# Performance work log

Measured on AMD Instinct MI355X. Metric: run time of the kernel, lower is better.

Reference implementation:

```python
import jax, jax.numpy as jnp
import numpy as np

NEG_SLOPE = 0.2  # PyG GATv2Conv default leaky_relu slope


def _gatv2(x, src, dst, eattr, Wl, bl, Wr, br, We, att, bias, N):
    """GATv2Conv (concat heads, eval mode -> no dropout).
    x: [N, Fin], src/dst: [E], eattr: [E, Fe], att: [H, C]."""
    H, C = att.shape
    xl = (x @ Wl.T + bl).reshape(N, H, C)   # lin_l -> source features
    xr = (x @ Wr.T + br).reshape(N, H, C)   # lin_r -> target features
    ea = (eattr @ We.T).reshape(-1, H, C)   # lin_edge (no bias)
    m = xl[src] + xr[dst] + ea              # [E, H, C]
    m = jnp.where(m >= 0, m, NEG_SLOPE * m)
    logits = jnp.einsum('ehc,hc->eh', m, att)  # [E, H]
    # segment softmax over incoming edges of each target node
    lmax = jax.ops.segment_max(logits, dst, num_segments=N)  # self-loops -> nonempty
    ex = jnp.exp(logits - lmax[dst])
    denom = jax.ops.segment_sum(ex, dst, num_segments=N)
    alpha = ex / denom[dst]                 # [E, H]
    out = jax.ops.segment_sum(alpha[:, :, None] * xl[src], dst, num_segments=N)
    return out.reshape(N, H * C) + bias


def setup_inputs() -> dict:
    key = jax.random.key(0)
    ks = jax.random.split(key, 24)
    B, num_nodes, Fn, Fe, deg = 16, 5000, 64, 16, 32
    N = B * num_nodes
    E = N * deg
    s = 0.05
    inp = {
        'x': jax.random.normal(ks[0], (N, Fn), jnp.float32),
        'edge_index': jax.random.randint(ks[1], (2, E), 0, N, jnp.int64),
        'edge_attr': jax.random.normal(ks[2], (E, Fe), jnp.float32),
        'num_nodes': num_nodes,
        'W1l': jax.random.normal(ks[3], (9, Fn), jnp.float32) * s,
        'b1l': jnp.zeros((9,), jnp.float32),
        'W1r': jax.random.normal(ks[4], (9, Fn), jnp.float32) * s,
        'b1r': jnp.zeros((9,), jnp.float32),
        'We1': jax.random.normal(ks[5], (9, Fe), jnp.float32) * s,
        'att1': jax.random.normal(ks[6], (3, 3), jnp.float32) * s,
        'bias1': jnp.zeros((9,), jnp.float32),
        'W2l': jax.random.normal(ks[7], (20, 9), jnp.float32) * s,
        'b2l': jnp.zeros((20,), jnp.float32),
        'W2r': jax.random.normal(ks[8], (20, 9), jnp.float32) * s,
        'b2r': jnp.zeros((20,), jnp.float32),
        'We2': jax.random.normal(ks[9], (20, Fe), jnp.float32) * s,
        'att2': jax.random.normal(ks[10], (4, 5), jnp.float32) * s,
        'bias2': jnp.zeros((20,), jnp.float32),
        'fcW1': jax.random.normal(ks[11], (100, 20 * num_nodes), jnp.float32) * 0.01,
        'fcb1': jnp.zeros((100,), jnp.float32),
        'fcW2': jax.random.normal(ks[12], (10, 100), jnp.float32) * s,
        'fcb2': jnp.zeros((10,), jnp.float32),
        'fcW3': jax.random.normal(ks[13], (1, 10), jnp.float32) * s,
        'fcb3': jnp.zeros((1,), jnp.float32),
    }
    return inp


def reference(x, edge_index, edge_attr, num_nodes,
              W1l, b1l, W1r, b1r, We1, att1, bias1,
              W2l, b2l, W2r, b2r, We2, att2, bias2,
              fcW1, fcb1, fcW2, fcb2, fcW3, fcb3):
    N = x.shape[0]
    src0, dst0 = edge_index[0], edge_index[1]
    # add_self_loops=True, fill_value='mean': loop attr = mean of incoming edge attrs
    cnt = jax.ops.segment_sum(jnp.ones((src0.shape[0],), x.dtype), dst0, num_segments=N)
    loop_attr = jax.ops.segment_sum(edge_attr, dst0, num_segments=N) / jnp.maximum(cnt, 1.0)[:, None]
    nodes = jnp.arange(N)
    src = jnp.concatenate([src0, nodes])
    dst = jnp.concatenate([dst0, nodes])
    ea = jnp.concatenate([edge_attr, loop_attr], axis=0)

    h = _gatv2(x, src, dst, ea, W1l, b1l, W1r, b1r, We1, att1, bias1, N)
    h = jax.nn.relu(h)
    h = _gatv2(h, src, dst, ea, W2l, b2l, W2r, b2r, We2, att2, bias2, N)
    h = jax.nn.relu(h)

    B = N // num_nodes
    h = h.reshape(B, num_nodes * 20)
    h = jax.nn.relu(h @ fcW1.T + fcb1)
    h = jax.nn.relu(h @ fcW2.T + fcb2)
    return h @ fcW3.T + fcb3
```

## Files before the change

kernel.cpp:

```cpp
#include <hip/hip_runtime.h>
#include <math.h>

#define TPB 256
#define CAP 96
#define CPAD 16

static inline int gridFor(size_t n) { return (int)((n + TPB - 1) / TPB); }


__global__ void __launch_bounds__(TPB) k_lin1(
    const float* __restrict__ x,
    const float* __restrict__ Wl, const float* __restrict__ bl,
    const float* __restrict__ Wr, const float* __restrict__ br,
    float* __restrict__ xl, float* __restrict__ xr, int N)
{
  int idx = blockIdx.x * TPB + threadIdx.x;
  if (idx >= N * 18) return;
  int i = idx / 18, t = idx % 18;
  bool left = t < 9;
  int j = left ? t : t - 9;
  const float* W = (left ? Wl : Wr) + j * 64;
  float s = (left ? bl : br)[j];
  const float* xi = x + (size_t)i * 64;
#pragma unroll
  for (int f = 0; f < 64; f++) s = fmaf(xi[f], W[f], s);
  (left ? xl : xr)[(size_t)i * 9 + j] = s;
}

__global__ void __launch_bounds__(TPB) k_lin2(
    const float* __restrict__ h1, const float* __restrict__ bias1,
    const float* __restrict__ Wl, const float* __restrict__ bl,
    const float* __restrict__ Wr, const float* __restrict__ br,
    float* __restrict__ xl, float* __restrict__ xr, int N)
{
  int idx = blockIdx.x * TPB + threadIdx.x;
  if (idx >= N * 40) return;
  int i = idx / 40, t = idx % 40;
  float hr[9];
#pragma unroll
  for (int k = 0; k < 9; k++) hr[k] = fmaxf(h1[(size_t)i * 9 + k] + bias1[k], 0.0f);
  bool left = t < 20;
  int j = left ? t : t - 20;
  const float* W = (left ? Wl : Wr) + j * 9;
  float s = (left ? bl : br)[j];
#pragma unroll
  for (int k = 0; k < 9; k++) s = fmaf(hr[k], W[k], s);
  (left ? xl : xr)[(size_t)i * 20 + j] = s;
}


__global__ void __launch_bounds__(TPB) k_scatter(
    const int* __restrict__ ei, int* __restrict__ cursor,
    int2* __restrict__ csr, int E)
{
  size_t e = (size_t)blockIdx.x * TPB + threadIdx.x;
  if (e >= (size_t)E) return;
  int src = ei[e];
  int dst = ei[(size_t)E + e];
  int slot = atomicAdd(&cursor[(size_t)dst * CPAD], 1);
  if (slot < CAP) csr[(size_t)dst * CAP + slot] = make_int2((int)e, src);
}


template <int H, int C>
__global__ void __launch_bounds__(TPB) k_attn(
    const int* __restrict__ cursor, const int2* __restrict__ csr,
    const float* __restrict__ eattr,
    const float* __restrict__ xl, const float* __restrict__ xr,
    const float* __restrict__ We, const float* __restrict__ att,
    const float* __restrict__ bias,
    float* __restrict__ out, int N)
{
  constexpr int HC = H * C;
  int idx = blockIdx.x * TPB + threadIdx.x;
  if (idx >= N * H) return;
  int n = idx / H, h = idx % H;

  float w[C][16];
#pragma unroll
  for (int c = 0; c < C; c++)
#pragma unroll
    for (int f = 0; f < 16; f++) w[c][f] = We[(h * C + c) * 16 + f];
  float attv[C], xrv[C];
#pragma unroll
  for (int c = 0; c < C; c++) {
    attv[c] = att[h * C + c];
    xrv[c] = xr[(size_t)n * HC + h * C + c];
  }

  int dg = cursor[(size_t)n * CPAD];
  int lim = min(dg, CAP);
  const int2* row = csr + (size_t)n * CAP;

  float mx = -INFINITY, den = 0.0f;
  float acc[C], ea_sum[C];
#pragma unroll
  for (int c = 0; c < C; c++) { acc[c] = 0.0f; ea_sum[c] = 0.0f; }

  for (int p = 0; p < lim; p++) {
    int2 es = row[p];
    float a[16];
    const float4* a4 = (const float4*)(eattr + (size_t)es.x * 16);
#pragma unroll
    for (int k = 0; k < 4; k++) {
      float4 v = a4[k];
      a[4 * k + 0] = v.x; a[4 * k + 1] = v.y; a[4 * k + 2] = v.z; a[4 * k + 3] = v.w;
    }
    const float* xs = xl + (size_t)es.y * HC + h * C;
    float xv[C];
#pragma unroll
    for (int c = 0; c < C; c++) xv[c] = xs[c];
    float lg = 0.0f;
#pragma unroll
    for (int c = 0; c < C; c++) {
      float ea = 0.0f;
#pragma unroll
      for (int f = 0; f < 16; f++) ea = fmaf(a[f], w[c][f], ea);
      ea_sum[c] += ea;
      float m = xv[c] + xrv[c] + ea;
      m = (m >= 0.0f) ? m : 0.2f * m;
      lg = fmaf(m, attv[c], lg);
    }
    float nm = fmaxf(mx, lg);
    float s = expf(mx - nm);
    float wE = expf(lg - nm);
    den = den * s + wE;
#pragma unroll
    for (int c = 0; c < C; c++) acc[c] = fmaf(acc[c], s, wE * xv[c]);
    mx = nm;
  }

  {
    float invd = 1.0f / fmaxf((float)dg, 1.0f);
    const float* xs = xl + (size_t)n * HC + h * C;
    float xv[C];
#pragma unroll
    for (int c = 0; c < C; c++) xv[c] = xs[c];
    float lg = 0.0f;
#pragma unroll
    for (int c = 0; c < C; c++) {
      float m = xv[c] + xrv[c] + ea_sum[c] * invd;
      m = (m >= 0.0f) ? m : 0.2f * m;
      lg = fmaf(m, attv[c], lg);
    }
    float nm = fmaxf(mx, lg);
    float s = expf(mx - nm);
    float wE = expf(lg - nm);
    den = den * s + wE;
#pragma unroll
    for (int c = 0; c < C; c++) acc[c] = fmaf(acc[c], s, wE * xv[c]);
  }

  float inv = 1.0f / den;
  float* od = out + (size_t)n * HC + h * C;
#pragma unroll
  for (int c = 0; c < C; c++) {
    float v = acc[c] * inv;
    if (bias) v = fmaxf(v + bias[h * C + c], 0.0f);
    od[c] = v;
  }
}


__global__ void __launch_bounds__(TPB) k_fc1(
    const float* __restrict__ h2, const float* __restrict__ W,
    float* __restrict__ h3, int NN, int Kc)
{
  int o = blockIdx.x;
  int ks = blockIdx.y;
  int k0 = ks * Kc;
  int k1 = min(NN, k0 + Kc);
  float acc[16];
#pragma unroll
  for (int b = 0; b < 16; b++) acc[b] = 0.0f;
  const float* wo = W + (size_t)o * NN;
  for (int k = k0 + threadIdx.x; k < k1; k += TPB) {
    float w = wo[k];
#pragma unroll
    for (int b = 0; b < 16; b++) acc[b] = fmaf(h2[(size_t)b * NN + k], w, acc[b]);
  }
#pragma unroll
  for (int b = 0; b < 16; b++) {
    float v = acc[b];
#pragma unroll
    for (int off = 32; off > 0; off >>= 1) v += __shfl_down(v, off, 64);
    if ((threadIdx.x & 63) == 0) atomicAdd(&h3[b * 100 + o], v);
  }
}

__global__ void __launch_bounds__(TPB) k_fc23(
    const float* __restrict__ h3, const float* __restrict__ fcb1,
    const float* __restrict__ W2, const float* __restrict__ b2,
    const float* __restrict__ W3, const float* __restrict__ b3,
    float* __restrict__ out, int B)
{
  __shared__ float s3[32 * 100];
  __shared__ float s4[32 * 10];
  int tid = threadIdx.x;
  for (int t = tid; t < B * 100; t += TPB)
    s3[t] = fmaxf(h3[t] + fcb1[t % 100], 0.0f);
  __syncthreads();
  if (tid < B * 10) {
    int b = tid / 10, o = tid % 10;
    float s = b2[o];
#pragma unroll
    for (int k = 0; k < 100; k++) s = fmaf(s3[b * 100 + k], W2[o * 100 + k], s);
    s4[tid] = fmaxf(s, 0.0f);
  }
  __syncthreads();
  if (tid < B) {
    float s = b3[0];
#pragma unroll
    for (int k = 0; k < 10; k++) s = fmaf(s4[tid * 10 + k], W3[k], s);
    out[tid] = s;
  }
}


extern "C" void kernel_launch(void* const* d_in, const int* in_sizes, int n_in,
                              void* d_out, int out_size, void* d_ws, size_t ws_size,
                              hipStream_t stream) {
  const float* x      = (const float*)d_in[0];
  const int*   ei     = (const int*)d_in[1];
  const float* eattr  = (const float*)d_in[2];
  const float* W1l = (const float*)d_in[4];  const float* b1l = (const float*)d_in[5];
  const float* W1r = (const float*)d_in[6];  const float* b1r = (const float*)d_in[7];
  const float* We1 = (const float*)d_in[8];  const float* att1 = (const float*)d_in[9];
  const float* bias1 = (const float*)d_in[10];
  const float* W2l = (const float*)d_in[11]; const float* b2l = (const float*)d_in[12];
  const float* W2r = (const float*)d_in[13]; const float* b2r = (const float*)d_in[14];
  const float* We2 = (const float*)d_in[15]; const float* att2 = (const float*)d_in[16];
  const float* bias2 = (const float*)d_in[17];
  const float* fcW1 = (const float*)d_in[18]; const float* fcb1 = (const float*)d_in[19];
  const float* fcW2 = (const float*)d_in[20]; const float* fcb2 = (const float*)d_in[21];
  const float* fcW3 = (const float*)d_in[22]; const float* fcb3 = (const float*)d_in[23];
  float* out = (float*)d_out;

  const int N = in_sizes[0] / 64;
  const int E = in_sizes[2] / 16;
  const int num_nodes = in_sizes[18] / (100 * 20);
  const int B = N / num_nodes;

  char* base = (char*)d_ws;
  size_t off = 0;
  auto alloc = [&](size_t bytes) {
    size_t o = off; off += (bytes + 63) & ~(size_t)63; return o;
  };
  size_t o_cursor = alloc((size_t)N * CPAD * 4);
  size_t o_h3     = alloc((size_t)B * 100 * 4);
  size_t zeroBytes = off;
  size_t o_csr    = alloc((size_t)N * CAP * 8);
  size_t o_xl1    = alloc((size_t)N * 9 * 4);
  size_t o_xr1    = alloc((size_t)N * 9 * 4);
  size_t o_xl2    = alloc((size_t)N * 20 * 4);
  size_t o_xr2    = alloc((size_t)N * 20 * 4);
  size_t o_h1     = alloc((size_t)N * 9 * 4);
  size_t o_h2     = alloc((size_t)N * 20 * 4);
  (void)ws_size;

  int*   cursor = (int*)(base + o_cursor);
  float* h3     = (float*)(base + o_h3);
  int2*  csr    = (int2*)(base + o_csr);
  float* xl1    = (float*)(base + o_xl1);
  float* xr1    = (float*)(base + o_xr1);
  float* xl2    = (float*)(base + o_xl2);
  float* xr2    = (float*)(base + o_xr2);
  float* h1     = (float*)(base + o_h1);
  float* h2     = (float*)(base + o_h2);

  hipMemsetAsync(d_ws, 0, zeroBytes, stream);

  k_lin1<<<gridFor((size_t)N * 18), TPB, 0, stream>>>(x, W1l, b1l, W1r, b1r, xl1, xr1, N);

  k_scatter<<<gridFor((size_t)E), TPB, 0, stream>>>(ei, cursor, csr, E);

  k_attn<3, 3><<<gridFor((size_t)N * 3), TPB, 0, stream>>>(
      cursor, csr, eattr, xl1, xr1, We1, att1, nullptr, h1, N);

  k_lin2<<<gridFor((size_t)N * 40), TPB, 0, stream>>>(h1, bias1, W2l, b2l, W2r, b2r, xl2, xr2, N);

  k_attn<4, 5><<<gridFor((size_t)N * 4), TPB, 0, stream>>>(
      cursor, csr, eattr, xl2, xr2, We2, att2, bias2, h2, N);

  const int NN = num_nodes * 20;
  const int KS = 16;
  const int Kc = (NN + KS - 1) / KS;
  dim3 g1(100, KS);
  k_fc1<<<g1, TPB, 0, stream>>>(h2, fcW1, h3, NN, Kc);
  k_fc23<<<1, TPB, 0, stream>>>(h3, fcb1, fcW2, fcb2, fcW3, fcb3, out, B);
  (void)out_size; (void)n_in;
}
```

Measured before the change: 856.5 us.

## Build compact CSR via two-level bucket sort and reorder edge attributes

Replaces the per-node atomic slot scatter into a fixed-capacity padded CSR with a two-level binning scheme. Edges are binned by destination block using shared-memory histograms, bucket offsets are scanned, and a per-bucket kernel builds a compact rowptr/src/eid CSR. When workspace allows, edge attributes are permuted into CSR order so the attention kernels read them sequentially instead of gathering by edge id. This adds several kernels and a full copy of the edge attributes. It relies on fixed bucket capacity (BCAP) and on edge ids fitting in 22 bits.

New measurement: 832.4 us. -2.8%, faster.

```diff
diff --git a/kernel.cpp b/kernel.cpp
--- a/kernel.cpp
+++ b/kernel.cpp
@@ -1,9 +1,12 @@
 #include <hip/hip_runtime.h>
 #include <math.h>
 
-#define TPB 256
-#define CAP 96
-#define CPAD 16
+#define TPB   256
+#define NPB   256
+#define MAXNB 512
+#define BCAP  10240
+#define ITEMS 32
+#define CPAD  16
 
 static inline int gridFor(size_t n) { return (int)((n + TPB - 1) / TPB); }
 
@@ -49,23 +52,122 @@
 }
 
 
-__global__ void __launch_bounds__(TPB) k_scatter(
-    const int* __restrict__ ei, int* __restrict__ cursor,
-    int2* __restrict__ csr, int E)
-{
-  size_t e = (size_t)blockIdx.x * TPB + threadIdx.x;
-  if (e >= (size_t)E) return;
-  int src = ei[e];
-  int dst = ei[(size_t)E + e];
-  int slot = atomicAdd(&cursor[(size_t)dst * CPAD], 1);
-  if (slot < CAP) csr[(size_t)dst * CAP + slot] = make_int2((int)e, src);
-}
-
-
-template <int H, int C>
+__global__ void __launch_bounds__(TPB) k_bin(
+    const int* __restrict__ ei, int* __restrict__ bucketCntP,
+    int2* __restrict__ staging, int E, int NB)
+{
+  __shared__ int hist[MAXNB];
+  __shared__ int base[MAXNB];
+  int tid = threadIdx.x;
+  size_t tile0 = (size_t)blockIdx.x * (TPB * ITEMS);
+  for (int i = tid; i < NB; i += TPB) hist[i] = 0;
+  __syncthreads();
+  for (int it = 0; it < ITEMS; ++it) {
+    size_t e = tile0 + (size_t)it * TPB + tid;
+    if (e < (size_t)E) {
+      int dst = ei[(size_t)E + e];
+      atomicAdd(&hist[dst >> 8], 1);
+    }
+  }
+  __syncthreads();
+  for (int i = tid; i < NB; i += TPB) {
+    int c = hist[i];
+    base[i] = c ? atomicAdd(&bucketCntP[(size_t)i * CPAD], c) : 0;
+    hist[i] = 0;
+  }
+  __syncthreads();
+  for (int it = 0; it < ITEMS; ++it) {
+    size_t e = tile0 + (size_t)it * TPB + tid;
+    if (e < (size_t)E) {
+      int src = ei[e];
+      int dst = ei[(size_t)E + e];
+      int b = dst >> 8;
+      int r = atomicAdd(&hist[b], 1);
+      staging[(size_t)b * BCAP + base[b] + r] =
+          make_int2((int)e | ((dst & 255) << 22), src);
+    }
+  }
+}
+
+
+__global__ void __launch_bounds__(MAXNB) k_scanb(
+    const int* __restrict__ bucketCntP, int* __restrict__ bucketBase, int NB)
+{
+  __shared__ int s[MAXNB];
+  int tid = threadIdx.x;
+  int v = (tid < NB) ? bucketCntP[(size_t)tid * CPAD] : 0;
+  s[tid] = v;
+  __syncthreads();
+  for (int off = 1; off < MAXNB; off <<= 1) {
+    int u = (tid >= off) ? s[tid - off] : 0;
+    __syncthreads();
+    s[tid] += u;
+    __syncthreads();
+  }
+  if (tid < NB) bucketBase[tid] = s[tid] - v;
+}
+
+
+__global__ void __launch_bounds__(TPB) k_csr(
+    const int2* __restrict__ staging, const int* __restrict__ bucketCntP,
+    const int* __restrict__ bucketBase,
+    int* __restrict__ rowptr, int* __restrict__ degO,
+    int* __restrict__ src_csr, int* __restrict__ eid_csr, int N)
+{
+  int b = blockIdx.x, tid = threadIdx.x;
+  int n0 = b << 8;
+  int recCnt = bucketCntP[(size_t)b * CPAD];
+  int ebase = bucketBase[b];
+  const int2* rec = staging + (size_t)b * BCAP;
+  __shared__ int deg_s[NPB];
+  __shared__ int pfx[NPB];
+  __shared__ int cur[NPB];
+  deg_s[tid] = 0;
+  __syncthreads();
+  for (int r = tid; r < recCnt; r += TPB)
+    atomicAdd(&deg_s[(rec[r].x >> 22) & 255], 1);
+  __syncthreads();
+  pfx[tid] = deg_s[tid];
+  __syncthreads();
+  for (int off = 1; off < NPB; off <<= 1) {
+    int u = (tid >= off) ? pfx[tid - off] : 0;
+    __syncthreads();
+    pfx[tid] += u;
+    __syncthreads();
+  }
+  int excl = pfx[tid] - deg_s[tid];
+  int n = n0 + tid;
+  if (n < N) { rowptr[n] = ebase + excl; degO[n] = deg_s[tid]; }
+  cur[tid] = ebase + excl;
+  __syncthreads();
+  for (int r = tid; r < recCnt; r += TPB) {
+    int2 rc = rec[r];
+    int dl = (rc.x >> 22) & 255;
+    int eid = rc.x & 0x3FFFFF;
+    int pos = atomicAdd(&cur[dl], 1);
+    src_csr[pos] = rc.y;
+    eid_csr[pos] = eid;
+  }
+}
+
+
+__global__ void __launch_bounds__(TPB) k_reorder(
+    const int* __restrict__ eid_csr, const float* __restrict__ eattr,
+    float4* __restrict__ eac, int E)
+{
+  int slot = blockIdx.x * TPB + threadIdx.x;
+  if (slot >= E) return;
+  const float4* s = (const float4*)(eattr + (size_t)eid_csr[slot] * 16);
+  float4* d = eac + (size_t)slot * 4;
+  d[0] = s[0]; d[1] = s[1]; d[2] = s[2]; d[3] = s[3];
+}
+
+
+template <int H, int C, bool SEQ>
 __global__ void __launch_bounds__(TPB) k_attn(
-    const int* __restrict__ cursor, const int2* __restrict__ csr,
-    const float* __restrict__ eattr,
+    const int* __restrict__ rowptr, const int* __restrict__ deg,
+    const int* __restrict__ src_csr, const int* __restrict__ eid_csr,
+    const float* __restrict__ ea_src,
     const float* __restrict__ xl, const float* __restrict__ xr,
     const float* __restrict__ We, const float* __restrict__ att,
     const float* __restrict__ bias,
@@ -88,25 +190,26 @@
     xrv[c] = xr[(size_t)n * HC + h * C + c];
   }
 
-  int dg = cursor[(size_t)n * CPAD];
-  int lim = min(dg, CAP);
-  const int2* row = csr + (size_t)n * CAP;
+  int r0 = rowptr[n];
+  int dg = deg[n];
 
   float mx = -INFINITY, den = 0.0f;
   float acc[C], ea_sum[C];
 #pragma unroll
   for (int c = 0; c < C; c++) { acc[c] = 0.0f; ea_sum[c] = 0.0f; }
 
-  for (int p = 0; p < lim; p++) {
-    int2 es = row[p];
+  for (int p = 0; p < dg; p++) {
+    int pos = r0 + p;
+    size_t abase = SEQ ? (size_t)pos * 16 : (size_t)eid_csr[pos] * 16;
     float a[16];
-    const float4* a4 = (const float4*)(eattr + (size_t)es.x * 16);
+    const float4* a4 = (const float4*)(ea_src + abase);
 #pragma unroll
     for (int k = 0; k < 4; k++) {
       float4 v = a4[k];
       a[4 * k + 0] = v.x; a[4 * k + 1] = v.y; a[4 * k + 2] = v.z; a[4 * k + 3] = v.w;
     }
-    const float* xs = xl + (size_t)es.y * HC + h * C;
+    int srcn = src_csr[pos];
+    const float* xs = xl + (size_t)srcn * HC + h * C;
     float xv[C];
 #pragma unroll
     for (int c = 0; c < C; c++) xv[c] = xs[c];
@@ -240,47 +343,73 @@
   const int E = in_sizes[2] / 16;
   const int num_nodes = in_sizes[18] / (100 * 20);
   const int B = N / num_nodes;
+  const int NB = (N + NPB - 1) / NPB;
 
   char* base = (char*)d_ws;
   size_t off = 0;
   auto alloc = [&](size_t bytes) {
     size_t o = off; off += (bytes + 63) & ~(size_t)63; return o;
   };
-  size_t o_cursor = alloc((size_t)N * CPAD * 4);
+  size_t o_bcnt   = alloc((size_t)NB * CPAD * 4);
   size_t o_h3     = alloc((size_t)B * 100 * 4);
   size_t zeroBytes = off;
-  size_t o_csr    = alloc((size_t)N * CAP * 8);
+  size_t o_bbase  = alloc((size_t)NB * 4);
+  size_t o_stage  = alloc((size_t)NB * BCAP * 8);
+  size_t o_rowptr = alloc((size_t)N * 4);
+  size_t o_deg    = alloc((size_t)N * 4);
+  size_t o_srcc   = alloc((size_t)E * 4);
+  size_t o_eidc   = alloc((size_t)E * 4);
   size_t o_xl1    = alloc((size_t)N * 9 * 4);
   size_t o_xr1    = alloc((size_t)N * 9 * 4);
   size_t o_xl2    = alloc((size_t)N * 20 * 4);
   size_t o_xr2    = alloc((size_t)N * 20 * 4);
   size_t o_h1     = alloc((size_t)N * 9 * 4);
   size_t o_h2     = alloc((size_t)N * 20 * 4);
-  (void)ws_size;
-
-  int*   cursor = (int*)(base + o_cursor);
+  size_t o_eac    = alloc((size_t)E * 16 * 4);
+  bool seq = (off <= ws_size);
+
+  int*   bcnt   = (int*)(base + o_bcnt);
   float* h3     = (float*)(base + o_h3);
-  int2*  csr    = (int2*)(base + o_csr);
+  int*   bbase  = (int*)(base + o_bbase);
+  int2*  stage  = (int2*)(base + o_stage);
+  int*   rowptr = (int*)(base + o_rowptr);
+  int*   deg    = (int*)(base + o_deg);
+  int*   srcc   = (int*)(base + o_srcc);
+  int*   eidc   = (int*)(base + o_eidc);
   float* xl1    = (float*)(base + o_xl1);
   float* xr1    = (float*)(base + o_xr1);
   float* xl2    = (float*)(base + o_xl2);
   float* xr2    = (float*)(base + o_xr2);
   float* h1     = (float*)(base + o_h1);
   float* h2     = (float*)(base + o_h2);
+  float* eac    = (float*)(base + o_eac);
 
   hipMemsetAsync(d_ws, 0, zeroBytes, stream);
 
   k_lin1<<<gridFor((size_t)N * 18), TPB, 0, stream>>>(x, W1l, b1l, W1r, b1r, xl1, xr1, N);
 
-  k_scatter<<<gridFor((size_t)E), TPB, 0, stream>>>(ei, cursor, csr, E);
-
-  k_attn<3, 3><<<gridFor((size_t)N * 3), TPB, 0, stream>>>(
-      cursor, csr, eattr, xl1, xr1, We1, att1, nullptr, h1, N);
+  int binBlocks = (int)(((size_t)E + TPB * ITEMS - 1) / (TPB * ITEMS));
+  k_bin<<<binBlocks, TPB, 0, stream>>>(ei, bcnt, stage, E, NB);
+  k_scanb<<<1, MAXNB, 0, stream>>>(bcnt, bbase, NB);
+  k_csr<<<NB, TPB, 0, stream>>>(stage, bcnt, bbase, rowptr, deg, srcc, eidc, N);
+  if (seq)
+    k_reorder<<<gridFor((size_t)E), TPB, 0, stream>>>(eidc, eattr, (float4*)eac, E);
+
+  if (seq)
+    k_attn<3, 3, true><<<gridFor((size_t)N * 3), TPB, 0, stream>>>(
+        rowptr, deg, srcc, eidc, eac, xl1, xr1, We1, att1, nullptr, h1, N);
+  else
+    k_attn<3, 3, false><<<gridFor((size_t)N * 3), TPB, 0, stream>>>(
+        rowptr, deg, srcc, eidc, eattr, xl1, xr1, We1, att1, nullptr, h1, N);
 
   k_lin2<<<gridFor((size_t)N * 40), TPB, 0, stream>>>(h1, bias1, W2l, b2l, W2r, b2r, xl2, xr2, N);
 
-  k_attn<4, 5><<<gridFor((size_t)N * 4), TPB, 0, stream>>>(
-      cursor, csr, eattr, xl2, xr2, We2, att2, bias2, h2, N);
+  if (seq)
+    k_attn<4, 5, true><<<gridFor((size_t)N * 4), TPB, 0, stream>>>(
+        rowptr, deg, srcc, eidc, eac, xl2, xr2, We2, att2, bias2, h2, N);
+  else
+    k_attn<4, 5, false><<<gridFor((size_t)N * 4), TPB, 0, stream>>>(
+        rowptr, deg, srcc, eidc, eattr, xl2, xr2, We2, att2, bias2, h2, N);
 
   const int NN = num_nodes * 20;
   const int KS = 16;
```
